# Kernel optimization log

Measured on AMD Instinct MI355X. Metric: run time of the kernel, lower is better.

## Reference

```python
import jax, jax.numpy as jnp
import numpy as np


def setup_inputs() -> dict:
    key = jax.random.key(0)
    k1, k2, k3, k4, k5 = jax.random.split(key, 5)
    b, c, k, h, w = 8, 512, 19, 128, 128
    x = jax.random.normal(k1, (b, c, h, w), dtype=jnp.float32)
    # mask_conv: 1x1 conv ichn->ochn (weight [k, c], bias [k])
    Wm = jax.random.normal(k2, (k, c), dtype=jnp.float32) * (1.0 / np.sqrt(c))
    bm = jax.random.normal(k3, (k,), dtype=jnp.float32) * 0.02
    # filter_conv: grouped 1x1 conv, groups=k -> per-class [c_out, c_in] matmul
    Wf = jax.random.normal(k4, (k, c, c), dtype=jnp.float32) * (1.0 / np.sqrt(c))
    bf = jax.random.normal(k5, (k, c), dtype=jnp.float32) * 0.02
    return {"x": x, "Wm": Wm, "bm": bm, "Wf": Wf, "bf": bf}


def reference(x, Wm, bm, Wf, bf):
    b, c, h, w = x.shape
    k = Wm.shape[0]
    # mask_conv (1x1) + sigmoid -> [b, k, h, w]
    pre_mask = jnp.einsum('bchw,kc->bkhw', x, Wm) + bm[None, :, None, None]
    mask = jax.nn.sigmoid(pre_mask)
    # masked pooling: bmm(mask [b,k,hw], feat [b,hw,c]) / (h*w) -> [b, k, c]
    class_feat = jnp.einsum('bkhw,bchw->bkc', mask, x) / (h * w)
    # grouped 1x1 filter_conv: per class k, [c_out, c_in] GEMM on class_feat
    filters = jnp.einsum('koc,bkc->bko', Wf, class_feat) + bf[None, :, :]  # [b, k, c]
    # per-sample dynamic 1x1 conv (groups=b) == batched GEMM over channels
    pred = jnp.einsum('bkc,bchw->bkhw', filters, x)
    return pred
```

## Files before the change

### kernel.cpp

```cpp
#include <hip/hip_runtime.h>
#include <math.h>

#define BB 8
#define CC 512
#define KK 19
#define HWHW 16384
#define INV_HW (1.0f/16384.0f)

typedef __attribute__((ext_vector_type(8))) short bf16x8;
typedef __attribute__((ext_vector_type(4))) short s16x4;
typedef __attribute__((ext_vector_type(4))) float f32x4;

__device__ __forceinline__ unsigned short f2bf(float f) {
    unsigned int u = __float_as_uint(f);
    u = (u + 0x7fffu + ((u >> 16) & 1u)) >> 16;
    return (unsigned short)u;
}

__device__ __forceinline__ unsigned int pk_bf16(float a, float b) {
    unsigned int r;
    asm("v_cvt_pk_bf16_f32 %0, %1, %2" : "=v"(r) : "v"(a), "v"(b));
    return r;
}

__global__ __launch_bounds__(256, 3) void k_s1(const float* __restrict__ x,
                                               const float* __restrict__ Wm,
                                               const float* __restrict__ bm,
                                               unsigned short* __restrict__ mask,
                                               unsigned short* __restrict__ xt4g) {
    __shared__ short wm[20 * CC];
    __shared__ short xt[2][128 * 64];
    const int tid = threadIdx.x;
    const int b = blockIdx.x >> 7;
    const int pt = blockIdx.x & 127;
    const int p0 = pt << 7;
    const float* xb = x + ((size_t)b * CC) * HWHW + p0;

    for (int u = tid; u < 20 * 128; u += 256) {
        const int k = u >> 7;
        const int c4 = (u & 127) << 2;
        float4 w = {0.f, 0.f, 0.f, 0.f};
        if (k < KK) w = *(const float4*)(Wm + k * CC + c4);
        s16x4 v = { (short)f2bf(w.x), (short)f2bf(w.y), (short)f2bf(w.z), (short)f2bf(w.w) };
        *(s16x4*)&wm[(k << 9) + (((c4 >> 3) ^ (k & 7)) << 3) + (c4 & 7)] = v;
    }

    const int wv = tid >> 6, ln = tid & 63;
    const int lm = ln & 15, q = ln >> 4;
    const f32x4 zz = {0.f, 0.f, 0.f, 0.f};
    f32x4 acc[2][2];
    acc[0][0] = zz; acc[0][1] = zz; acc[1][0] = zz; acc[1][1] = zz;

    const int cg0 = tid >> 5;
    const int pA  = (tid & 31) << 2;
    const float* sA = xb + (size_t)(cg0 << 2) * HWHW + pA;
    const float* sB = xb + (size_t)((cg0 + 8) << 2) * HWHW + pA;
    unsigned short* t4fix = xt4g + ((size_t)((b << 7) | pt) << 16);

    float4 Fa[8], Fb[8];
#pragma unroll
    for (int j = 0; j < 4; ++j) {
        Fa[j]     = *(const float4*)(sA + (size_t)j * HWHW);
        Fa[4 + j] = *(const float4*)(sB + (size_t)j * HWHW);
    }

#pragma unroll
    for (int cs = 0; cs < 8; ++cs) {
        const float4* cur = (cs & 1) ? Fb : Fa;
        float4* nxt = (cs & 1) ? Fa : Fb;
        if (cs < 7) {
            const size_t co = (size_t)((cs + 1) << 6) * HWHW;
#pragma unroll
            for (int j = 0; j < 4; ++j) {
                nxt[j]     = *(const float4*)(sA + co + (size_t)j * HWHW);
                nxt[4 + j] = *(const float4*)(sB + co + (size_t)j * HWHW);
            }
        }
        short* xts = (short*)xt[cs & 1];
#pragma unroll
        for (int h = 0; h < 2; ++h) {
            const int cg = cg0 + (h << 3);
            const float* G0 = (const float*)&cur[(h << 2) + 0];
            const float* G1 = (const float*)&cur[(h << 2) + 1];
            const float* G2 = (const float*)&cur[(h << 2) + 2];
            const float* G3 = (const float*)&cur[(h << 2) + 3];
#pragma unroll
            for (int j = 0; j < 4; ++j) {
                const int pr = pA + j;
                uint2 v = make_uint2(pk_bf16(G0[j], G1[j]), pk_bf16(G2[j], G3[j]));
                const int idx = (pr << 6) + (((cg >> 1) ^ (pr & 7)) << 3) + ((cg & 1) << 2);
                *(uint2*)&xts[idx] = v;
            }
        }
        asm volatile("s_waitcnt lgkmcnt(0)" ::: "memory");
        __builtin_amdgcn_s_barrier();
        asm volatile("" ::: "memory");
#pragma unroll
        for (int ks = 0; ks < 2; ++ks) {
            const int gch = (cs << 3) + (ks << 2) + q;
            const int m1 = (lm < 3) ? (16 + lm) : 19;
            bf16x8 a0 = *(const bf16x8*)&wm[(lm << 9) + ((gch ^ (lm & 7)) << 3)];
            bf16x8 a1 = *(const bf16x8*)&wm[(m1 << 9) + ((gch ^ (m1 & 7)) << 3)];
            const int lch = (ks << 2) + q;
#pragma unroll
            for (int nt = 0; nt < 2; ++nt) {
                const int pr = (((wv << 1) + nt) << 4) + lm;
                bf16x8 bv = *(const bf16x8*)&xts[(pr << 6) + ((lch ^ (pr & 7)) << 3)];
                acc[0][nt] = __builtin_amdgcn_mfma_f32_16x16x32_bf16(a0, bv, acc[0][nt], 0, 0, 0);
                acc[1][nt] = __builtin_amdgcn_mfma_f32_16x16x32_bf16(a1, bv, acc[1][nt], 0, 0, 0);
            }
        }
        {
            unsigned short* t4 = t4fix + ((size_t)cs << 13);
#pragma unroll
            for (int r = 0; r < 4; ++r) {
                uint4 v = *(const uint4*)&xts[(r << 11) + (tid << 3)];
                *(uint4*)(t4 + (r << 11) + (tid << 3)) = v;
            }
        }
    }

    unsigned short* mb = mask + ((size_t)b * KK) * HWHW + p0;
#pragma unroll
    for (int mt = 0; mt < 2; ++mt)
#pragma unroll
        for (int r = 0; r < 4; ++r) {
            const int k = (mt << 4) + (q << 2) + r;
            if (k < KK) {
                const float bias = bm[k];
#pragma unroll
                for (int nt = 0; nt < 2; ++nt) {
                    const int p = (((wv << 1) + nt) << 4) + lm;
                    const float t = acc[mt][nt][r] + bias;
                    mb[(size_t)k * HWHW + p] = f2bf(1.0f / (1.0f + __expf(-t)));
                }
            }
        }
}

__global__ __launch_bounds__(256, 3) void k_s2(const unsigned short* __restrict__ xt4g,
                                               const unsigned short* __restrict__ mask,
                                               float* __restrict__ cf_part) {
    __shared__ short xls[2][8192];
    __shared__ short mtl[2][20 * 128];
    const int tid = threadIdx.x;
    const int cs = blockIdx.x & 7;
    const int ptg = (blockIdx.x >> 3) & 15;
    const int b = blockIdx.x >> 7;
    const int wv = tid >> 6, ln = tid & 63;
    const int lm = ln & 15, q = ln >> 4;

    const unsigned short* mb = mask + ((size_t)b * KK) * HWHW + (ptg << 10);
    const unsigned short* tbase = xt4g + (((size_t)(((b << 4) | ptg) << 6) + cs) << 13);

    const int mu1 = tid + 256;
    const int k0 = tid >> 4, ch0 = tid & 15;
    const int k1 = mu1 >> 4, ch1 = mu1 & 15;

    const f32x4 zz = {0.f, 0.f, 0.f, 0.f};
    f32x4 acc[2];
    acc[0] = zz; acc[1] = zz;

    uint4 Xa[4], Xb[4], Ma[2], Mb[2];
    const uint4 z4 = make_uint4(0u, 0u, 0u, 0u);

#pragma unroll
    for (int r = 0; r < 4; ++r) Xa[r] = *(const uint4*)(tbase + (r << 11) + (tid << 3));
    Ma[0] = z4; Ma[1] = z4;
    if (k0 < KK) Ma[0] = *(const uint4*)(mb + (size_t)k0 * HWHW + (ch0 << 3));
    if (mu1 < 320 && k1 < KK) Ma[1] = *(const uint4*)(mb + (size_t)k1 * HWHW + (ch1 << 3));

#pragma unroll
    for (int t = 0; t < 8; ++t) {
        const uint4* curX = (t & 1) ? Xb : Xa;
        uint4* nxtX = (t & 1) ? Xa : Xb;
        const uint4* curM = (t & 1) ? Mb : Ma;
        uint4* nxtM = (t & 1) ? Ma : Mb;
        if (t < 7) {
            const unsigned short* tp = tbase + ((size_t)(t + 1) << 16);
#pragma unroll
            for (int r = 0; r < 4; ++r) nxtX[r] = *(const uint4*)(tp + (r << 11) + (tid << 3));
            nxtM[0] = z4; nxtM[1] = z4;
            if (k0 < KK) nxtM[0] = *(const uint4*)(mb + (size_t)k0 * HWHW + ((t + 1) << 7) + (ch0 << 3));
            if (mu1 < 320 && k1 < KK) nxtM[1] = *(const uint4*)(mb + (size_t)k1 * HWHW + ((t + 1) << 7) + (ch1 << 3));
        }
        short* xl = (short*)xls[t & 1];
        short* ml = (short*)mtl[t & 1];
#pragma unroll
        for (int r = 0; r < 4; ++r) *(uint4*)&xl[(r << 11) + (tid << 3)] = curX[r];
        *(uint4*)&ml[(k0 << 7) + ((ch0 ^ (k0 & 7)) << 3)] = curM[0];
        if (mu1 < 320)
            *(uint4*)&ml[(k1 << 7) + ((ch1 ^ (k1 & 7)) << 3)] = curM[1];
        asm volatile("s_waitcnt lgkmcnt(0)" ::: "memory");
        __builtin_amdgcn_s_barrier();
        asm volatile("" ::: "memory");
        const int c = (wv << 4) + lm;
        const int m1 = (lm < 3) ? (16 + lm) : 19;
#pragma unroll
        for (int cc = 0; cc < 4; ++cc) {
            const int pb = (cc << 5) + (q << 3);
            short e[8];
#pragma unroll
            for (int i = 0; i < 8; ++i)
                e[i] = xl[((pb + i) << 6) + (((c >> 3) ^ i) << 3) + (c & 7)];
            bf16x8 bv = {e[0], e[1], e[2], e[3], e[4], e[5], e[6], e[7]};
            const int pg = (cc << 2) + q;
            bf16x8 a0 = *(const bf16x8*)&ml[(lm << 7) + ((pg ^ (lm & 7)) << 3)];
            bf16x8 a1 = *(const bf16x8*)&ml[(m1 << 7) + ((pg ^ (m1 & 7)) << 3)];
            acc[0] = __builtin_amdgcn_mfma_f32_16x16x32_bf16(a0, bv, acc[0], 0, 0, 0);
            acc[1] = __builtin_amdgcn_mfma_f32_16x16x32_bf16(a1, bv, acc[1], 0, 0, 0);
        }
    }

    float* dst = cf_part + ((size_t)(ptg * BB + b) * KK) * CC + (cs << 6) + (wv << 4) + lm;
#pragma unroll
    for (int mt = 0; mt < 2; ++mt)
#pragma unroll
        for (int r = 0; r < 4; ++r) {
            const int k = (mt << 4) + (q << 2) + r;
            if (k < KK) dst[(size_t)k * CC] = acc[mt][r];
        }
}

__global__ __launch_bounds__(256) void k_s2r(const float* __restrict__ part,
                                             float* __restrict__ cf) {
    const int i = blockIdx.x * 256 + threadIdx.x;
    if (i >= BB * KK * CC) return;
    const int b = i / (KK * CC);
    const int rem = i - b * (KK * CC);
    float sum = 0.0f;
#pragma unroll
    for (int s = 0; s < 16; ++s)
        sum += part[((size_t)(s * BB + b) * KK) * CC + rem];
    cf[i] = sum * INV_HW;
}

__global__ __launch_bounds__(256) void k_filters(const float* __restrict__ Wf,
                                                 const float* __restrict__ bf,
                                                 const float* __restrict__ cf,
                                                 float* __restrict__ fil) {
    const int blk = blockIdx.x;
    const int k = blk >> 7;
    const int o = ((blk & 127) << 2) + (threadIdx.x >> 6);
    const int lane = threadIdx.x & 63;
    const float* wrow = Wf + ((size_t)k * CC + o) * CC;

    float acc[BB];
#pragma unroll
    for (int b = 0; b < BB; ++b) acc[b] = 0.0f;
#pragma unroll
    for (int j = 0; j < CC / 64; ++j) {
        const int c = lane + (j << 6);
        const float wv = wrow[c];
#pragma unroll
        for (int b = 0; b < BB; ++b)
            acc[b] += wv * cf[((size_t)b * KK + k) * CC + c];
    }
#pragma unroll
    for (int b = 0; b < BB; ++b) {
#pragma unroll
        for (int off = 32; off > 0; off >>= 1)
            acc[b] += __shfl_down(acc[b], off, 64);
    }
    if (lane == 0) {
        const float bias = bf[k * CC + o];
#pragma unroll
        for (int b = 0; b < BB; ++b)
            fil[((size_t)b * KK + k) * CC + o] = acc[b] + bias;
    }
}

__global__ __launch_bounds__(256, 3) void k_s4(const unsigned short* __restrict__ xt4g,
                                               const float* __restrict__ fil,
                                               float* __restrict__ out) {
    __shared__ short wm[20 * CC];
    __shared__ short xt[2][128 * 64];
    const int tid = threadIdx.x;
    const int b = blockIdx.x >> 7;
    const int pt = blockIdx.x & 127;
    const int p0 = pt << 7;
    const float* fb = fil + ((size_t)b * KK) * CC;
    const unsigned short* tb = xt4g + ((size_t)((b << 7) | pt) << 16);

    for (int u = tid; u < 20 * 128; u += 256) {
        const int k = u >> 7;
        const int c4 = (u & 127) << 2;
        float4 w = {0.f, 0.f, 0.f, 0.f};
        if (k < KK) w = *(const float4*)(fb + k * CC + c4);
        s16x4 v = { (short)f2bf(w.x), (short)f2bf(w.y), (short)f2bf(w.z), (short)f2bf(w.w) };
        *(s16x4*)&wm[(k << 9) + (((c4 >> 3) ^ (k & 7)) << 3) + (c4 & 7)] = v;
    }

    const int wv = tid >> 6, ln = tid & 63;
    const int lm = ln & 15, q = ln >> 4;
    const f32x4 zz = {0.f, 0.f, 0.f, 0.f};
    f32x4 acc[2][2];
    acc[0][0] = zz; acc[0][1] = zz; acc[1][0] = zz; acc[1][1] = zz;

    uint4 Ta[4], Tb4[4];
#pragma unroll
    for (int r = 0; r < 4; ++r)
        Ta[r] = *(const uint4*)(tb + (r << 11) + (tid << 3));

#pragma unroll
    for (int cs = 0; cs < 8; ++cs) {
        const uint4* cur = (cs & 1) ? Tb4 : Ta;
        uint4* nxt = (cs & 1) ? Ta : Tb4;
        if (cs < 7) {
#pragma unroll
            for (int r = 0; r < 4; ++r)
                nxt[r] = *(const uint4*)(tb + ((size_t)(cs + 1) << 13) + (r << 11) + (tid << 3));
        }
        short* xts = (short*)xt[cs & 1];
#pragma unroll
        for (int r = 0; r < 4; ++r)
            *(uint4*)&xts[(r << 11) + (tid << 3)] = cur[r];
        asm volatile("s_waitcnt lgkmcnt(0)" ::: "memory");
        __builtin_amdgcn_s_barrier();
        asm volatile("" ::: "memory");
#pragma unroll
        for (int ks = 0; ks < 2; ++ks) {
            const int gch = (cs << 3) + (ks << 2) + q;
            const int m1 = (lm < 3) ? (16 + lm) : 19;
            bf16x8 a0 = *(const bf16x8*)&wm[(lm << 9) + ((gch ^ (lm & 7)) << 3)];
            bf16x8 a1 = *(const bf16x8*)&wm[(m1 << 9) + ((gch ^ (m1 & 7)) << 3)];
            const int lch = (ks << 2) + q;
#pragma unroll
            for (int nt = 0; nt < 2; ++nt) {
                const int pr = (((wv << 1) + nt) << 4) + lm;
                bf16x8 bv = *(const bf16x8*)&xts[(pr << 6) + ((lch ^ (pr & 7)) << 3)];
                acc[0][nt] = __builtin_amdgcn_mfma_f32_16x16x32_bf16(a0, bv, acc[0][nt], 0, 0, 0);
                acc[1][nt] = __builtin_amdgcn_mfma_f32_16x16x32_bf16(a1, bv, acc[1][nt], 0, 0, 0);
            }
        }
    }

    float* ob = out + ((size_t)b * KK) * HWHW + p0;
#pragma unroll
    for (int mt = 0; mt < 2; ++mt)
#pragma unroll
        for (int r = 0; r < 4; ++r) {
            const int k = (mt << 4) + (q << 2) + r;
            if (k < KK) {
#pragma unroll
                for (int nt = 0; nt < 2; ++nt) {
                    const int p = (((wv << 1) + nt) << 4) + lm;
                    ob[(size_t)k * HWHW + p] = acc[mt][nt][r];
                }
            }
        }
}

extern "C" void kernel_launch(void* const* d_in, const int* in_sizes, int n_in,
                              void* d_out, int out_size, void* d_ws, size_t ws_size,
                              hipStream_t stream) {
    const float* x  = (const float*)d_in[0];
    const float* Wm = (const float*)d_in[1];
    const float* bm = (const float*)d_in[2];
    const float* Wf = (const float*)d_in[3];
    const float* bf = (const float*)d_in[4];
    float* out = (float*)d_out;

    char* p = (char*)d_ws;
    unsigned short* mask = (unsigned short*)p;  p += (size_t)BB * KK * HWHW * 2;
    float* cf_part = (float*)p;                 p += (size_t)16 * BB * KK * CC * 4;
    float* cf  = (float*)p;                     p += (size_t)BB * KK * CC * 4;
    float* fil = (float*)p;                     p += (size_t)BB * KK * CC * 4;
    unsigned short* xt4g = (unsigned short*)p;

    k_s1<<<1024, 256, 0, stream>>>(x, Wm, bm, mask, xt4g);
    k_s2<<<1024, 256, 0, stream>>>(xt4g, mask, cf_part);
    k_s2r<<<(BB * KK * CC + 255) / 256, 256, 0, stream>>>(cf_part, cf);
    k_filters<<<KK * 128, 256, 0, stream>>>(Wf, bf, cf, fil);
    k_s4<<<1024, 256, 0, stream>>>(xt4g, fil, out);
}
```

Measured before the change: 460.2 us.

## Fuse mask computation and masked pooling into one kernel keeping tile in LDS

Merges the mask-conv kernel and the masked-pooling kernel into a single 512-thread kernel. The whole bf16 x tile (128 pixels by 512 channels) stays in LDS, and the sigmoid mask is written to LDS rather than global memory. The pooling GEMM is then done locally, which removes the global mask round-trip and the second read of the transposed x. In exchange, each tile writes a per-pixel-tile partial, so the partial buffer grows eightfold (128 partials instead of 16) and the reduction kernel does more work. The roughly 160KB LDS footprint also limits occupancy, and prefetch changes to triple-buffered register loads.

```diff
diff --git a/kernel.cpp b/kernel.cpp
--- a/kernel.cpp
+++ b/kernel.cpp
@@ -23,20 +23,34 @@
     return r;
 }
 
-__global__ __launch_bounds__(256, 3) void k_s1(const float* __restrict__ x,
-                                               const float* __restrict__ Wm,
-                                               const float* __restrict__ bm,
-                                               unsigned short* __restrict__ mask,
-                                               unsigned short* __restrict__ xt4g) {
+__global__ __launch_bounds__(512, 2) void k_s12(const float* __restrict__ x,
+                                                const float* __restrict__ Wm,
+                                                const float* __restrict__ bm,
+                                                float* __restrict__ cf_part,
+                                                unsigned short* __restrict__ xt4g) {
     __shared__ short wm[20 * CC];
-    __shared__ short xt[2][128 * 64];
+    __shared__ short xf[8 * 8192];
+    __shared__ short mlds[20 * 128];
     const int tid = threadIdx.x;
     const int b = blockIdx.x >> 7;
     const int pt = blockIdx.x & 127;
-    const int p0 = pt << 7;
-    const float* xb = x + ((size_t)b * CC) * HWHW + p0;
-
-    for (int u = tid; u < 20 * 128; u += 256) {
+    const float* xb = x + ((size_t)b * CC) * HWHW + (pt << 7);
+
+    const int wv = tid >> 6, ln = tid & 63;
+    const int lm = ln & 15, q = ln >> 4;
+
+    const int cr0 = (tid >> 5) << 2;
+    const int pA = (tid & 31) << 2;
+    const int cg = tid >> 5;
+    const float* sbase = xb + (size_t)cr0 * HWHW + pA;
+
+    float4 Fa[4], Fb[4], Fc[4];
+#pragma unroll
+    for (int j = 0; j < 4; ++j) Fa[j] = *(const float4*)(sbase + (size_t)j * HWHW);
+#pragma unroll
+    for (int j = 0; j < 4; ++j) Fb[j] = *(const float4*)(sbase + (size_t)(64 + j) * HWHW);
+
+    for (int u = tid; u < 20 * 128; u += 512) {
         const int k = u >> 7;
         const int c4 = (u & 127) << 2;
         float4 w = {0.f, 0.f, 0.f, 0.f};
@@ -44,57 +58,39 @@
         s16x4 v = { (short)f2bf(w.x), (short)f2bf(w.y), (short)f2bf(w.z), (short)f2bf(w.w) };
         *(s16x4*)&wm[(k << 9) + (((c4 >> 3) ^ (k & 7)) << 3) + (c4 & 7)] = v;
     }
-
-    const int wv = tid >> 6, ln = tid & 63;
-    const int lm = ln & 15, q = ln >> 4;
+    if (tid < 16)
+        *(uint4*)&mlds[(19 << 7) + (tid << 3)] = make_uint4(0u, 0u, 0u, 0u);
+
     const f32x4 zz = {0.f, 0.f, 0.f, 0.f};
-    f32x4 acc[2][2];
-    acc[0][0] = zz; acc[0][1] = zz; acc[1][0] = zz; acc[1][1] = zz;
-
-    const int cg0 = tid >> 5;
-    const int pA  = (tid & 31) << 2;
-    const float* sA = xb + (size_t)(cg0 << 2) * HWHW + pA;
-    const float* sB = xb + (size_t)((cg0 + 8) << 2) * HWHW + pA;
+    f32x4 acc[2];
+    acc[0] = zz; acc[1] = zz;
+
     unsigned short* t4fix = xt4g + ((size_t)((b << 7) | pt) << 16);
 
-    float4 Fa[8], Fb[8];
-#pragma unroll
-    for (int j = 0; j < 4; ++j) {
-        Fa[j]     = *(const float4*)(sA + (size_t)j * HWHW);
-        Fa[4 + j] = *(const float4*)(sB + (size_t)j * HWHW);
-    }
-
 #pragma unroll
     for (int cs = 0; cs < 8; ++cs) {
-        const float4* cur = (cs & 1) ? Fb : Fa;
-        float4* nxt = (cs & 1) ? Fa : Fb;
-        if (cs < 7) {
-            const size_t co = (size_t)((cs + 1) << 6) * HWHW;
-#pragma unroll
-            for (int j = 0; j < 4; ++j) {
-                nxt[j]     = *(const float4*)(sA + co + (size_t)j * HWHW);
-                nxt[4 + j] = *(const float4*)(sB + co + (size_t)j * HWHW);
-            }
-        }
-        short* xts = (short*)xt[cs & 1];
-#pragma unroll
-        for (int h = 0; h < 2; ++h) {
-            const int cg = cg0 + (h << 3);
-            const float* G0 = (const float*)&cur[(h << 2) + 0];
-            const float* G1 = (const float*)&cur[(h << 2) + 1];
-            const float* G2 = (const float*)&cur[(h << 2) + 2];
-            const float* G3 = (const float*)&cur[(h << 2) + 3];
-#pragma unroll
-            for (int j = 0; j < 4; ++j) {
-                const int pr = pA + j;
-                uint2 v = make_uint2(pk_bf16(G0[j], G1[j]), pk_bf16(G2[j], G3[j]));
-                const int idx = (pr << 6) + (((cg >> 1) ^ (pr & 7)) << 3) + ((cg & 1) << 2);
-                *(uint2*)&xts[idx] = v;
-            }
-        }
-        asm volatile("s_waitcnt lgkmcnt(0)" ::: "memory");
-        __builtin_amdgcn_s_barrier();
-        asm volatile("" ::: "memory");
+        const float4* cur = (cs % 3 == 0) ? Fa : ((cs % 3 == 1) ? Fb : Fc);
+        float4* nxt = ((cs + 2) % 3 == 0) ? Fa : (((cs + 2) % 3 == 1) ? Fb : Fc);
+        if (cs < 6) {
+            const size_t co = (size_t)((cs + 2) << 6) * HWHW;
+#pragma unroll
+            for (int j = 0; j < 4; ++j)
+                nxt[j] = *(const float4*)(sbase + co + (size_t)j * HWHW);
+        }
+        short* xts = &xf[cs << 13];
+        {
+            const float* G0 = (const float*)&cur[0];
+            const float* G1 = (const float*)&cur[1];
+            const float* G2 = (const float*)&cur[2];
+            const float* G3 = (const float*)&cur[3];
+#pragma unroll
+            for (int jj = 0; jj < 4; ++jj) {
+                const int pr = pA + jj;
+                uint2 v = make_uint2(pk_bf16(G0[jj], G1[jj]), pk_bf16(G2[jj], G3[jj]));
+                *(uint2*)&xts[(pr << 6) + (((cg >> 1) ^ (pr & 7)) << 3) + ((cg & 1) << 2)] = v;
+            }
+        }
+        __syncthreads();
 #pragma unroll
         for (int ks = 0; ks < 2; ++ks) {
             const int gch = (cs << 3) + (ks << 2) + q;
@@ -102,123 +98,78 @@
             bf16x8 a0 = *(const bf16x8*)&wm[(lm << 9) + ((gch ^ (lm & 7)) << 3)];
             bf16x8 a1 = *(const bf16x8*)&wm[(m1 << 9) + ((gch ^ (m1 & 7)) << 3)];
             const int lch = (ks << 2) + q;
-#pragma unroll
-            for (int nt = 0; nt < 2; ++nt) {
-                const int pr = (((wv << 1) + nt) << 4) + lm;
-                bf16x8 bv = *(const bf16x8*)&xts[(pr << 6) + ((lch ^ (pr & 7)) << 3)];
-                acc[0][nt] = __builtin_amdgcn_mfma_f32_16x16x32_bf16(a0, bv, acc[0][nt], 0, 0, 0);
-                acc[1][nt] = __builtin_amdgcn_mfma_f32_16x16x32_bf16(a1, bv, acc[1][nt], 0, 0, 0);
-            }
+            const int pr = (wv << 4) + lm;
+            bf16x8 bv = *(const bf16x8*)&xts[(pr << 6) + ((lch ^ (pr & 7)) << 3)];
+            acc[0] = __builtin_amdgcn_mfma_f32_16x16x32_bf16(a0, bv, acc[0], 0, 0, 0);
+            acc[1] = __builtin_amdgcn_mfma_f32_16x16x32_bf16(a1, bv, acc[1], 0, 0, 0);
         }
         {
             unsigned short* t4 = t4fix + ((size_t)cs << 13);
 #pragma unroll
+            for (int r = 0; r < 2; ++r) {
+                uint4 v = *(const uint4*)&xts[(r << 12) + (tid << 3)];
+                *(uint4*)(t4 + (r << 12) + (tid << 3)) = v;
+            }
+        }
+        __syncthreads();
+    }
+
+    {
+        const int prow = (wv << 4) + lm;
+#pragma unroll
+        for (int mt = 0; mt < 2; ++mt)
+#pragma unroll
             for (int r = 0; r < 4; ++r) {
-                uint4 v = *(const uint4*)&xts[(r << 11) + (tid << 3)];
-                *(uint4*)(t4 + (r << 11) + (tid << 3)) = v;
-            }
-        }
-    }
-
-    unsigned short* mb = mask + ((size_t)b * KK) * HWHW + p0;
+                const int k = (mt << 4) + (q << 2) + r;
+                if (k < KK) {
+                    const float t = acc[mt][r] + bm[k];
+                    const unsigned short mv = f2bf(1.0f / (1.0f + __expf(-t)));
+                    mlds[(k << 7) + (((prow >> 3) ^ (k & 7)) << 3) + (prow & 7)] =
+                        (short)mv;
+                }
+            }
+    }
+    __syncthreads();
+
+    f32x4 pacc[2][4];
+#pragma unroll
+    for (int mt = 0; mt < 2; ++mt)
+#pragma unroll
+        for (int ct = 0; ct < 4; ++ct) pacc[mt][ct] = zz;
+
+    const short* xw = &xf[wv << 13];
+    const int m1 = (lm < 3) ? (16 + lm) : 19;
+#pragma unroll
+    for (int kp = 0; kp < 4; ++kp) {
+        const int pg = (kp << 2) + q;
+        bf16x8 a0 = *(const bf16x8*)&mlds[(lm << 7) + ((pg ^ (lm & 7)) << 3)];
+        bf16x8 a1 = *(const bf16x8*)&mlds[(m1 << 7) + ((pg ^ (m1 & 7)) << 3)];
+#pragma unroll
+        for (int ct = 0; ct < 4; ++ct) {
+            const int cl = (ct << 4) + lm;
+            short e[8];
+#pragma unroll
+            for (int i = 0; i < 8; ++i) {
+                const int p = (kp << 5) + (q << 3) + i;
+                e[i] = xw[(p << 6) + (((cl >> 3) ^ (p & 7)) << 3) + (cl & 7)];
+            }
+            bf16x8 bv = {e[0], e[1], e[2], e[3], e[4], e[5], e[6], e[7]};
+            pacc[0][ct] = __builtin_amdgcn_mfma_f32_16x16x32_bf16(a0, bv, pacc[0][ct], 0, 0, 0);
+            pacc[1][ct] = __builtin_amdgcn_mfma_f32_16x16x32_bf16(a1, bv, pacc[1][ct], 0, 0, 0);
+        }
+    }
+
+    float* dst = cf_part + ((size_t)pt * BB + b) * KK * CC;
 #pragma unroll
     for (int mt = 0; mt < 2; ++mt)
 #pragma unroll
         for (int r = 0; r < 4; ++r) {
             const int k = (mt << 4) + (q << 2) + r;
             if (k < KK) {
-                const float bias = bm[k];
-#pragma unroll
-                for (int nt = 0; nt < 2; ++nt) {
-                    const int p = (((wv << 1) + nt) << 4) + lm;
-                    const float t = acc[mt][nt][r] + bias;
-                    mb[(size_t)k * HWHW + p] = f2bf(1.0f / (1.0f + __expf(-t)));
-                }
-            }
-        }
-}
-
-__global__ __launch_bounds__(256, 3) void k_s2(const unsigned short* __restrict__ xt4g,
-                                               const unsigned short* __restrict__ mask,
-                                               float* __restrict__ cf_part) {
-    __shared__ short xls[2][8192];
-    __shared__ short mtl[2][20 * 128];
-    const int tid = threadIdx.x;
-    const int cs = blockIdx.x & 7;
-    const int ptg = (blockIdx.x >> 3) & 15;
-    const int b = blockIdx.x >> 7;
-    const int wv = tid >> 6, ln = tid & 63;
-    const int lm = ln & 15, q = ln >> 4;
-
-    const unsigned short* mb = mask + ((size_t)b * KK) * HWHW + (ptg << 10);
-    const unsigned short* tbase = xt4g + (((size_t)(((b << 4) | ptg) << 6) + cs) << 13);
-
-    const int mu1 = tid + 256;
-    const int k0 = tid >> 4, ch0 = tid & 15;
-    const int k1 = mu1 >> 4, ch1 = mu1 & 15;
-
-    const f32x4 zz = {0.f, 0.f, 0.f, 0.f};
-    f32x4 acc[2];
-    acc[0] = zz; acc[1] = zz;
-
-    uint4 Xa[4], Xb[4], Ma[2], Mb[2];
-    const uint4 z4 = make_uint4(0u, 0u, 0u, 0u);
-
-#pragma unroll
-    for (int r = 0; r < 4; ++r) Xa[r] = *(const uint4*)(tbase + (r << 11) + (tid << 3));
-    Ma[0] = z4; Ma[1] = z4;
-    if (k0 < KK) Ma[0] = *(const uint4*)(mb + (size_t)k0 * HWHW + (ch0 << 3));
-    if (mu1 < 320 && k1 < KK) Ma[1] = *(const uint4*)(mb + (size_t)k1 * HWHW + (ch1 << 3));
-
-#pragma unroll
-    for (int t = 0; t < 8; ++t) {
-        const uint4* curX = (t & 1) ? Xb : Xa;
-        uint4* nxtX = (t & 1) ? Xa : Xb;
-        const uint4* curM = (t & 1) ? Mb : Ma;
-        uint4* nxtM = (t & 1) ? Ma : Mb;
-        if (t < 7) {
-            const unsigned short* tp = tbase + ((size_t)(t + 1) << 16);
-#pragma unroll
-            for (int r = 0; r < 4; ++r) nxtX[r] = *(const uint4*)(tp + (r << 11) + (tid << 3));
-            nxtM[0] = z4; nxtM[1] = z4;
-            if (k0 < KK) nxtM[0] = *(const uint4*)(mb + (size_t)k0 * HWHW + ((t + 1) << 7) + (ch0 << 3));
-            if (mu1 < 320 && k1 < KK) nxtM[1] = *(const uint4*)(mb + (size_t)k1 * HWHW + ((t + 1) << 7) + (ch1 << 3));
-        }
-        short* xl = (short*)xls[t & 1];
-        short* ml = (short*)mtl[t & 1];
-#pragma unroll
-        for (int r = 0; r < 4; ++r) *(uint4*)&xl[(r << 11) + (tid << 3)] = curX[r];
-        *(uint4*)&ml[(k0 << 7) + ((ch0 ^ (k0 & 7)) << 3)] = curM[0];
-        if (mu1 < 320)
-            *(uint4*)&ml[(k1 << 7) + ((ch1 ^ (k1 & 7)) << 3)] = curM[1];
-        asm volatile("s_waitcnt lgkmcnt(0)" ::: "memory");
-        __builtin_amdgcn_s_barrier();
-        asm volatile("" ::: "memory");
-        const int c = (wv << 4) + lm;
-        const int m1 = (lm < 3) ? (16 + lm) : 19;
-#pragma unroll
-        for (int cc = 0; cc < 4; ++cc) {
-            const int pb = (cc << 5) + (q << 3);
-            short e[8];
-#pragma unroll
-            for (int i = 0; i < 8; ++i)
-                e[i] = xl[((pb + i) << 6) + (((c >> 3) ^ i) << 3) + (c & 7)];
-            bf16x8 bv = {e[0], e[1], e[2], e[3], e[4], e[5], e[6], e[7]};
-            const int pg = (cc << 2) + q;
-            bf16x8 a0 = *(const bf16x8*)&ml[(lm << 7) + ((pg ^ (lm & 7)) << 3)];
-            bf16x8 a1 = *(const bf16x8*)&ml[(m1 << 7) + ((pg ^ (m1 & 7)) << 3)];
-            acc[0] = __builtin_amdgcn_mfma_f32_16x16x32_bf16(a0, bv, acc[0], 0, 0, 0);
-            acc[1] = __builtin_amdgcn_mfma_f32_16x16x32_bf16(a1, bv, acc[1], 0, 0, 0);
-        }
-    }
-
-    float* dst = cf_part + ((size_t)(ptg * BB + b) * KK) * CC + (cs << 6) + (wv << 4) + lm;
-#pragma unroll
-    for (int mt = 0; mt < 2; ++mt)
-#pragma unroll
-        for (int r = 0; r < 4; ++r) {
-            const int k = (mt << 4) + (q << 2) + r;
-            if (k < KK) dst[(size_t)k * CC] = acc[mt][r];
+#pragma unroll
+                for (int ct = 0; ct < 4; ++ct)
+                    dst[k * CC + (wv << 6) + (ct << 4) + lm] = pacc[mt][ct][r];
+            }
         }
 }
 
@@ -229,9 +180,9 @@
     const int b = i / (KK * CC);
     const int rem = i - b * (KK * CC);
     float sum = 0.0f;
-#pragma unroll
-    for (int s = 0; s < 16; ++s)
-        sum += part[((size_t)(s * BB + b) * KK) * CC + rem];
+#pragma unroll 8
+    for (int pt = 0; pt < 128; ++pt)
+        sum += part[((size_t)pt * BB + b) * KK * CC + rem];
     cf[i] = sum * INV_HW;
 }
 
@@ -362,14 +313,12 @@
     float* out = (float*)d_out;
 
     char* p = (char*)d_ws;
-    unsigned short* mask = (unsigned short*)p;  p += (size_t)BB * KK * HWHW * 2;
-    float* cf_part = (float*)p;                 p += (size_t)16 * BB * KK * CC * 4;
+    float* cf_part = (float*)p;                 p += (size_t)128 * BB * KK * CC * 4;
     float* cf  = (float*)p;                     p += (size_t)BB * KK * CC * 4;
     float* fil = (float*)p;                     p += (size_t)BB * KK * CC * 4;
     unsigned short* xt4g = (unsigned short*)p;
 
-    k_s1<<<1024, 256, 0, stream>>>(x, Wm, bm, mask, xt4g);
-    k_s2<<<1024, 256, 0, stream>>>(xt4g, mask, cf_part);
+    k_s12<<<1024, 512, 0, stream>>>(x, Wm, bm, cf_part, xt4g);
     k_s2r<<<(BB * KK * CC + 255) / 256, 256, 0, stream>>>(cf_part, cf);
     k_filters<<<KK * 128, 256, 0, stream>>>(Wf, bf, cf, fil);
     k_s4<<<1024, 256, 0, stream>>>(xt4g, fil, out);
```

Result: faster. 449.9 us (-2.2%).
